# Kernel optimization log

Hardware: AMD Instinct MI355X
Metric: run time of the kernel (lower is better)

The kernel has to match this reference:

```python
import jax, jax.numpy as jnp
import numpy as np

# Fuzzy convolution (gaussian membership, 'prod' T-norm):
# firing_r(patch) = prod_{ki,kj,c} exp(-0.5*((x-mu_{r,c})*sigma_{ki,kj,c,r})^2)
#                 = exp(-0.5 * sum_{ki,kj,c} ((x-mu)*sigma)^2)
# The quadratic expands so the whole premise stage is two VALID convolutions:
#   sum (x^2)*s2 - 2*sum x*(mu*s2) + sum (mu^2)*s2,  with s2 = sigma^2.

_DN = ('NHWC', 'HWIO', 'NHWC')

def _conv(a, k):
    return jax.lax.conv_general_dilated(a, k, window_strides=(1, 1), padding='VALID', dimension_numbers=_DN)

def _firing(x, sigma, mu):
    # x: (B,H,W,C); sigma: (kh,kw,C,R); mu: (R,C)
    s2 = sigma * sigma                              # (kh,kw,C,R)
    mu_cr = mu.T[None, None, :, :]                  # (1,1,C,R)
    quad = _conv(x * x, s2) - 2.0 * _conv(x, s2 * mu_cr)  # (B,H',W',R)
    const = jnp.sum(s2 * mu_cr * mu_cr, axis=(0, 1, 2))   # (R,)
    return jnp.exp(-0.5 * (quad + const))           # (B,H',W',R)

def setup_inputs() -> dict:
    key = jax.random.key(0)
    k1, k2, k3, k4 = jax.random.split(key, 4)
    B, H, W, C = 32, 256, 256, 32
    R, O = 8, 16
    x = jax.random.normal(k1, (B, H, W, C), dtype=jnp.float32)
    # small positive sigmas keep sum over 3*3*32 window terms O(1) so firing is not ~0
    premise_sigma = 0.1 * jax.random.uniform(k2, (3, 3, C, R), dtype=jnp.float32)
    premise_mu = jax.random.normal(k3, (R, C), dtype=jnp.float32)
    residual = jnp.full((1,), 0.01, dtype=jnp.float32)  # Constant(0.01) initializer
    consequent_bias = jax.random.normal(k4, (R + 1, O), dtype=jnp.float32)
    return {"x": x, "premise_sigma": premise_sigma, "premise_mu": premise_mu,
            "residual": residual, "consequent_bias": consequent_bias}

def reference(x, premise_sigma, premise_mu, residual, consequent_bias):
    phi = _firing(x, premise_sigma, premise_mu)                     # (B,H',W',R)
    res = jnp.broadcast_to(residual, phi.shape[:-1] + (1,))         # residual rule
    phi = jnp.concatenate([phi, res], axis=-1)                      # (B,H',W',R+1)
    phi_norm = phi / (jnp.sum(phi, axis=-1, keepdims=True) + 1e-9)  # normalized firing
    # constant-output-MF consequent combine: rules -> outputs
    return jnp.einsum('bhwr,ro->bhwo', phi_norm, consequent_bias)   # (B,H',W',O)
```

## Files before the change

kernel.cpp:

```cpp
#include <hip/hip_runtime.h>


#define CIN 32
#define HH  256
#define WW  256
#define HO  254
#define WO  254
#define BB  32
#define OO  16

#define TW 64
#define TH 8
#define LROWS 10
#define LPIX 66
#define ROWCH (LPIX * 4)
#define LDS_CHUNKS (LROWS * ROWCH)
#define STAGE_ITERS 11
#define NTILE (4 * 32 * BB)

typedef _Float16 half8 __attribute__((ext_vector_type(8)));
typedef float f32x4 __attribute__((ext_vector_type(4)));

static __device__ __forceinline__ unsigned short f2h(float f) {
    _Float16 h = (_Float16)f;
    return *reinterpret_cast<unsigned short*>(&h);
}

__global__ __launch_bounds__(256) void prep_kernel(const float* __restrict__ sigma,
                                                   const float* __restrict__ mu,
                                                   unsigned short* __restrict__ wb,
                                                   float* __restrict__ Kc) {
    const int tid = threadIdx.x;
    for (int item = tid; item < 18 * 64; item += 256) {
        const int frag = item >> 6;
        const int lane = item & 63;
        const int tap = frag >> 1, ftype = frag & 1;
        const int n = lane & 15, g = lane >> 4;
#pragma unroll
        for (int e = 0; e < 8; ++e) {
            float wgt = 0.f;
            if (n < 8) {
                const int c = g * 8 + e;
                const float sg = sigma[(tap * CIN + c) * 8 + n];
                const float s2 = sg * sg;
                wgt = ftype ? -0.5f * s2 : s2 * mu[n * CIN + c];
            }
            wb[item * 8 + e] = f2h(wgt);
        }
    }
    if (tid < 8) {
        const int r = tid;
        float k = 0.f;
        for (int item = 0; item < 9 * CIN; ++item) {
            const int c = item & 31;
            const float sg = sigma[item * 8 + r];
            const float m = mu[r * CIN + c];
            k = fmaf(sg * sg, m * m, k);
        }
        Kc[r] = -0.5f * k;
    }
}

__global__ __launch_bounds__(256, 3) void fuzzy_main(const float* __restrict__ x,
                                                     const unsigned short* __restrict__ wb,
                                                     const float* __restrict__ Kc,
                                                     const float* __restrict__ residual,
                                                     const float* __restrict__ cb,
                                                     float* __restrict__ out) {
    __shared__ __align__(16) unsigned char ldsRaw[LDS_CHUNKS * 16];
    half8* ldsH = reinterpret_cast<half8*>(ldsRaw);

    const int tid = threadIdx.x;
    const int lin  = blockIdx.x;
    const int tile = ((lin & 7) << 9) | (lin >> 3);
    const int jt = tile & 3;
    const int it = (tile >> 2) & 31;
    const int b  = tile >> 7;
    const int i0 = min(TH * it, HO - TH);
    const int j0 = min(TW * jt, WO - TW);

    float4 va[STAGE_ITERS], vb[STAGE_ITERS];
#pragma unroll
    for (int t = 0; t < STAGE_ITERS; ++t) {
        const int f = tid + t * 256;
        const int fc = min(f, LDS_CHUNKS - 1);
        const int row = fc / ROWCH;
        const int rem = fc - row * ROWCH;
        const float4* src = reinterpret_cast<const float4*>(
            x + (((size_t)b * HH + (size_t)(i0 + row)) * WW + (size_t)j0) * CIN);
        va[t] = src[2 * rem];
        vb[t] = src[2 * rem + 1];
    }
#pragma unroll
    for (int t = 0; t < STAGE_ITERS; ++t) {
        const int f = tid + t * 256;
        if (f < LDS_CHUNKS) {
            const int row = f / ROWCH;
            const int rem = f - row * ROWCH;
            const int px = rem >> 2, gg = rem & 3;
            half8 h;
            h[0] = (_Float16)va[t].x; h[1] = (_Float16)va[t].y;
            h[2] = (_Float16)va[t].z; h[3] = (_Float16)va[t].w;
            h[4] = (_Float16)vb[t].x; h[5] = (_Float16)vb[t].y;
            h[6] = (_Float16)vb[t].z; h[7] = (_Float16)vb[t].w;
            ldsH[row * ROWCH + (px << 2) + (gg ^ (px & 3))] = h;
        }
    }

    const int lane = tid & 63;
    const int m = lane & 15, g = lane >> 4;

    const half8* wbv = reinterpret_cast<const half8*>(wb);
    half8 Bf[18];
#pragma unroll
    for (int q = 0; q < 18; ++q) Bf[q] = wbv[q * 64 + lane];

    const float res = residual[0];
    const float4 kc4 = reinterpret_cast<const float4*>(Kc)[g & 1];
    half8 a2;
#pragma unroll
    for (int e = 0; e < 8; ++e) {
        const int r = g * 8 + e;
        const float w = cb[min(r, 8) * OO + m];
        a2[e] = (_Float16)((r <= 8) ? w : 0.f);
    }
    unsigned resw;
    { unsigned short rb = f2h(res); resw = (unsigned)rb; }

    __syncthreads();

    const int wv_ = tid >> 6;

    int bc[3];
#pragma unroll
    for (int kj = 0; kj < 3; ++kj) {
        const int p = m + kj;
        bc[kj] = (p << 2) + (g ^ (p & 3));
    }

#pragma unroll
    for (int half = 0; half < 2; ++half) {
        const int row0 = wv_ + 4 * half;

        f32x4 acc[4];
#pragma unroll
        for (int nt = 0; nt < 4; ++nt) acc[nt] = (f32x4){0.f, 0.f, 0.f, 0.f};

        const half8* baseS = ldsH + row0 * ROWCH;
#pragma unroll
        for (int ki = 0; ki < 3; ++ki) {
#pragma unroll
            for (int kj = 0; kj < 3; ++kj) {
                const int tap = ki * 3 + kj;
                half8 ax[4];
#pragma unroll
                for (int nt = 0; nt < 4; ++nt)
                    ax[nt] = baseS[ki * ROWCH + nt * 64 + bc[kj]];
#pragma unroll
                for (int nt = 0; nt < 4; ++nt)
                    acc[nt] = __builtin_amdgcn_mfma_f32_16x16x32_f16(Bf[2 * tap], ax[nt], acc[nt], 0, 0, 0);
#pragma unroll
                for (int nt = 0; nt < 4; ++nt) {
                    const half8 ax2 = ax[nt] * ax[nt];
                    acc[nt] = __builtin_amdgcn_mfma_f32_16x16x32_f16(Bf[2 * tap + 1], ax2, acc[nt], 0, 0, 0);
                }
            }
        }

        const size_t orow = ((size_t)b * HO + (size_t)(i0 + wv_ + 4 * half)) * WO + (size_t)j0;
#pragma unroll
        for (int nt = 0; nt < 4; ++nt) {
            float phv[4];
#pragma unroll
            for (int e = 0; e < 4; ++e) {
                const float t = __expf(acc[nt][e] + ((const float*)&kc4)[e]);
                phv[e] = (g < 2) ? t : 0.f;
            }
            const float S = (phv[0] + phv[1]) + (phv[2] + phv[3]);
            const float T = S + __shfl_xor(S, 16);
            const float denom = T + __shfl_xor(T, 32) + res + 1e-9f;
            const float inv = __builtin_amdgcn_rcpf(denom);

            const unsigned w01 = (unsigned)f2h(phv[0]) | ((unsigned)f2h(phv[1]) << 16);
            const unsigned w23 = (unsigned)f2h(phv[2]) | ((unsigned)f2h(phv[3]) << 16);
            const unsigned p01 = __shfl_xor(w01, 16);
            const unsigned p23 = __shfl_xor(w23, 16);
            uint4 bw;
            bw.x = (g == 0) ? w01 : ((g == 1) ? resw : 0u);
            bw.y = (g == 0) ? w23 : 0u;
            bw.z = (g == 0) ? p01 : 0u;
            bw.w = (g == 0) ? p23 : 0u;
            const half8 b2 = __builtin_bit_cast(half8, bw);

            f32x4 acc2 = (f32x4){0.f, 0.f, 0.f, 0.f};
            acc2 = __builtin_amdgcn_mfma_f32_16x16x32_f16(a2, b2, acc2, 0, 0, 0);

            f32x4 v;
            v[0] = acc2[0] * inv; v[1] = acc2[1] * inv;
            v[2] = acc2[2] * inv; v[3] = acc2[3] * inv;
            float* op = out + (orow + (size_t)(nt * 16 + m)) * OO + g * 4;
            __builtin_nontemporal_store(v, reinterpret_cast<f32x4*>(op));
        }
    }
}

extern "C" void kernel_launch(void* const* d_in, const int* in_sizes, int n_in,
                              void* d_out, int out_size, void* d_ws, size_t ws_size,
                              hipStream_t stream) {
    const float* x     = (const float*)d_in[0];
    const float* sigma = (const float*)d_in[1];
    const float* mu    = (const float*)d_in[2];
    const float* resid = (const float*)d_in[3];
    const float* cb    = (const float*)d_in[4];
    float* outp = (float*)d_out;

    float* Kc = (float*)d_ws;
    unsigned short* wb = (unsigned short*)(Kc + 8);

    hipLaunchKernelGGL(prep_kernel, dim3(1), dim3(256), 0, stream, sigma, mu, wb, Kc);
    hipLaunchKernelGGL(fuzzy_main, dim3(NTILE), dim3(256), 0, stream,
                       x, wb, Kc, resid, cb, outp);
}
```

Measured before the change: 86.34 us.

## Split LDS staging so the second row block overlaps first-half MFMA compute

Staging of the input tile is split into two parts. The first six LDS rows are written before the first barrier. The remaining four rows are held in registers and written to LDS after the first half's MFMA loop, followed by a second barrier before the second half. This lets the first half start compute sooner while the later loads are still in flight. It also replaces the elementwise float-to-half conversion with packed round-toward-zero conversion (cvt_pkrtz), which changes rounding slightly and adds a barrier plus register pressure.

Measured after the change: 104.0 us. 1.2x slower.

```diff
diff --git a/kernel.cpp b/kernel.cpp
--- a/kernel.cpp
+++ b/kernel.cpp
@@ -15,15 +15,27 @@
 #define LPIX 66
 #define ROWCH (LPIX * 4)
 #define LDS_CHUNKS (LROWS * ROWCH)
-#define STAGE_ITERS 11
+#define ACH (6 * ROWCH)
+#define AIT 7
+#define BIT 5
 #define NTILE (4 * 32 * BB)
 
 typedef _Float16 half8 __attribute__((ext_vector_type(8)));
+typedef _Float16 half2v __attribute__((ext_vector_type(2)));
 typedef float f32x4 __attribute__((ext_vector_type(4)));
 
 static __device__ __forceinline__ unsigned short f2h(float f) {
     _Float16 h = (_Float16)f;
     return *reinterpret_cast<unsigned short*>(&h);
+}
+
+static __device__ __forceinline__ half8 pack_pkrtz(const float4& a, const float4& b) {
+    uint4 u;
+    u.x = __builtin_bit_cast(unsigned, __builtin_amdgcn_cvt_pkrtz(a.x, a.y));
+    u.y = __builtin_bit_cast(unsigned, __builtin_amdgcn_cvt_pkrtz(a.z, a.w));
+    u.z = __builtin_bit_cast(unsigned, __builtin_amdgcn_cvt_pkrtz(b.x, b.y));
+    u.w = __builtin_bit_cast(unsigned, __builtin_amdgcn_cvt_pkrtz(b.z, b.w));
+    return __builtin_bit_cast(half8, u);
 }
 
 __global__ __launch_bounds__(256) void prep_kernel(const float* __restrict__ sigma,
@@ -79,41 +91,43 @@
     const int i0 = min(TH * it, HO - TH);
     const int j0 = min(TW * jt, WO - TW);
 
-    float4 va[STAGE_ITERS], vb[STAGE_ITERS];
-#pragma unroll
-    for (int t = 0; t < STAGE_ITERS; ++t) {
+    const float4* xbase = reinterpret_cast<const float4*>(
+        x + (((size_t)b * HH + (size_t)i0) * WW + (size_t)j0) * CIN);
+
+    float4 va[AIT], vb[AIT];
+#pragma unroll
+    for (int t = 0; t < AIT; ++t) {
+        const int f = min(tid + t * 256, ACH - 1);
+        const int row = f / ROWCH, rem = f - row * ROWCH;
+        va[t] = xbase[(size_t)row * 2048 + 2 * rem];
+        vb[t] = xbase[(size_t)row * 2048 + 2 * rem + 1];
+    }
+    float4 wa[BIT], wbv4[BIT];
+#pragma unroll
+    for (int t = 0; t < BIT; ++t) {
+        const int f = min(ACH + tid + t * 256, LDS_CHUNKS - 1);
+        const int row = f / ROWCH, rem = f - row * ROWCH;
+        wa[t] = xbase[(size_t)row * 2048 + 2 * rem];
+        wbv4[t] = xbase[(size_t)row * 2048 + 2 * rem + 1];
+    }
+
+#pragma unroll
+    for (int t = 0; t < AIT; ++t) {
         const int f = tid + t * 256;
-        const int fc = min(f, LDS_CHUNKS - 1);
-        const int row = fc / ROWCH;
-        const int rem = fc - row * ROWCH;
-        const float4* src = reinterpret_cast<const float4*>(
-            x + (((size_t)b * HH + (size_t)(i0 + row)) * WW + (size_t)j0) * CIN);
-        va[t] = src[2 * rem];
-        vb[t] = src[2 * rem + 1];
-    }
-#pragma unroll
-    for (int t = 0; t < STAGE_ITERS; ++t) {
-        const int f = tid + t * 256;
-        if (f < LDS_CHUNKS) {
-            const int row = f / ROWCH;
-            const int rem = f - row * ROWCH;
+        if (f < ACH) {
+            const int row = f / ROWCH, rem = f - row * ROWCH;
             const int px = rem >> 2, gg = rem & 3;
-            half8 h;
-            h[0] = (_Float16)va[t].x; h[1] = (_Float16)va[t].y;
-            h[2] = (_Float16)va[t].z; h[3] = (_Float16)va[t].w;
-            h[4] = (_Float16)vb[t].x; h[5] = (_Float16)vb[t].y;
-            h[6] = (_Float16)vb[t].z; h[7] = (_Float16)vb[t].w;
-            ldsH[row * ROWCH + (px << 2) + (gg ^ (px & 3))] = h;
+            ldsH[row * ROWCH + (px << 2) + (gg ^ (px & 3))] = pack_pkrtz(va[t], vb[t]);
         }
     }
 
     const int lane = tid & 63;
     const int m = lane & 15, g = lane >> 4;
 
-    const half8* wbv = reinterpret_cast<const half8*>(wb);
+    const half8* wbp = reinterpret_cast<const half8*>(wb);
     half8 Bf[18];
 #pragma unroll
-    for (int q = 0; q < 18; ++q) Bf[q] = wbv[q * 64 + lane];
+    for (int q = 0; q < 18; ++q) Bf[q] = wbp[q * 64 + lane];
 
     const float res = residual[0];
     const float4 kc4 = reinterpret_cast<const float4*>(Kc)[g & 1];
@@ -167,7 +181,19 @@
             }
         }
 
-        const size_t orow = ((size_t)b * HO + (size_t)(i0 + wv_ + 4 * half)) * WO + (size_t)j0;
+        if (half == 0) {
+#pragma unroll
+            for (int t = 0; t < BIT; ++t) {
+                const int f = ACH + tid + t * 256;
+                if (f < LDS_CHUNKS) {
+                    const int row = f / ROWCH, rem = f - row * ROWCH;
+                    const int px = rem >> 2, gg = rem & 3;
+                    ldsH[row * ROWCH + (px << 2) + (gg ^ (px & 3))] = pack_pkrtz(wa[t], wbv4[t]);
+                }
+            }
+        }
+
+        const size_t orow = ((size_t)b * HO + (size_t)(i0 + row0)) * WO + (size_t)j0;
 #pragma unroll
         for (int nt = 0; nt < 4; ++nt) {
             float phv[4];
@@ -201,6 +227,8 @@
             float* op = out + (orow + (size_t)(nt * 16 + m)) * OO + g * 4;
             __builtin_nontemporal_store(v, reinterpret_cast<f32x4*>(op));
         }
+
+        if (half == 0) __syncthreads();
     }
 }
 
```
